# Kernel tuning notes

Measured on AMD Instinct MI355X. Metric: run time of the kernel, lower is better.

The kernel has to match this reference:

```python
import jax, jax.numpy as jnp
import numpy as np

B, N, F, UNITS = 8, 4096, 128, 64
NEG = -1e10
LEAKY_SLOPE = 0.2  # tf.nn.leaky_relu default


def setup_inputs() -> dict:
    key = jax.random.key(0)
    k1, k2, k3, k4, k5 = jax.random.split(key, 5)
    H = jax.random.normal(k1, (B, N, F), dtype=jnp.float32)
    A = jax.random.randint(k2, (B, N, N), 0, 2).astype(jnp.float32)
    # self-loops so every row has at least one unmasked entry
    A = jnp.maximum(A, jnp.eye(N, dtype=jnp.float32)[None])
    W = jax.random.normal(k3, (F, UNITS), dtype=jnp.float32) * (1.0 / np.sqrt(F))
    a_1 = jax.random.normal(k4, (UNITS, 1), dtype=jnp.float32) * (1.0 / np.sqrt(UNITS))
    a_2 = jax.random.normal(k5, (UNITS, 1), dtype=jnp.float32) * (1.0 / np.sqrt(UNITS))
    return {"H": H, "A": A, "W": W, "a_1": a_1, "a_2": a_2}


def reference(H, A, W, a_1, a_2):
    X = H @ W                                  # [B, N, U]
    attn_self = X @ a_1                        # [B, N, 1]
    attn_neigh = X @ a_2                       # [B, N, 1]
    attention = attn_self + jnp.swapaxes(attn_neigh, 1, 2)   # [B, N, N]
    E = jax.nn.leaky_relu(attention, negative_slope=LEAKY_SLOPE)
    masked_E = E + NEG * (1.0 - A)
    alpha = jax.nn.softmax(masked_E, axis=-1)  # row-wise softmax
    H_cap = alpha @ X                          # [B, N, U]
    return jax.nn.relu(H_cap)
```

## Files before the change

kernel.cpp:

```cpp
#include <hip/hip_runtime.h>
#include <hip/hip_bf16.h>


#define NTOK 4096
#define FDIM 128
#define UDIM 64
#define BATCH 8

typedef __attribute__((ext_vector_type(8))) short short8;
typedef __attribute__((ext_vector_type(4))) float f32x4;

__device__ __forceinline__ unsigned short f2bf(float x) {
    unsigned u = __float_as_uint(x);
    return (unsigned short)((u + 0x7fffu + ((u >> 16) & 1u)) >> 16);
}

__global__ __launch_bounds__(256) void prep_kernel(
    const float* __restrict__ H,
    const float* __restrict__ W,
    const float* __restrict__ a1,
    const float* __restrict__ a2,
    unsigned short* __restrict__ XT,
    float* __restrict__ s_out,
    float* __restrict__ t_out)
{
    __shared__ float Xl[4][16][UDIM + 1];

    const int tid  = threadIdx.x;
    const int wave = tid >> 6, lane = tid & 63;
    const int col  = lane & 15, quad = lane >> 4;
    const int i0   = (blockIdx.x * 4 + wave) * 16;

    f32x4 acc0 = {0,0,0,0}, acc1 = {0,0,0,0}, acc2 = {0,0,0,0}, acc3 = {0,0,0,0};
    const float* hrow = H + (size_t)(i0 + col) * FDIM + quad * 8;

    #pragma unroll
    for (int kb = 0; kb < FDIM; kb += 32) {
        f32x4 h0 = *(const f32x4*)(hrow + kb);
        f32x4 h1 = *(const f32x4*)(hrow + kb + 4);
        short8 afr, b0, b1, b2, b3;
        #pragma unroll
        for (int j = 0; j < 4; ++j) {
            afr[j]     = (short)f2bf(h0[j]);
            afr[4 + j] = (short)f2bf(h1[j]);
        }
        #pragma unroll
        for (int j = 0; j < 8; ++j) {
            int k = kb + quad * 8 + j;
            b0[j] = (short)f2bf(W[k * UDIM + col]);
            b1[j] = (short)f2bf(W[k * UDIM + 16 + col]);
            b2[j] = (short)f2bf(W[k * UDIM + 32 + col]);
            b3[j] = (short)f2bf(W[k * UDIM + 48 + col]);
        }
        acc0 = __builtin_amdgcn_mfma_f32_16x16x32_bf16(afr, b0, acc0, 0, 0, 0);
        acc1 = __builtin_amdgcn_mfma_f32_16x16x32_bf16(afr, b1, acc1, 0, 0, 0);
        acc2 = __builtin_amdgcn_mfma_f32_16x16x32_bf16(afr, b2, acc2, 0, 0, 0);
        acc3 = __builtin_amdgcn_mfma_f32_16x16x32_bf16(afr, b3, acc3, 0, 0, 0);
    }
    #pragma unroll
    for (int r = 0; r < 4; ++r) {
        Xl[wave][quad * 4 + r][col]      = acc0[r];
        Xl[wave][quad * 4 + r][16 + col] = acc1[r];
        Xl[wave][quad * 4 + r][32 + col] = acc2[r];
        Xl[wave][quad * 4 + r][48 + col] = acc3[r];
    }
    __syncthreads();

    const int b = i0 >> 12, n0 = i0 & (NTOK - 1);
    float ps = 0.f, pt = 0.f;
    #pragma unroll
    for (int ui = 0; ui < 16; ++ui) {
        int u = quad * 16 + ui;
        float x = Xl[wave][col][u];
        ps = fmaf(x, a1[u], ps);
        pt = fmaf(x, a2[u], pt);
    }
    ps += __shfl_xor(ps, 16, 64); ps += __shfl_xor(ps, 32, 64);
    pt += __shfl_xor(pt, 16, 64); pt += __shfl_xor(pt, 32, 64);
    if (quad == 0) s_out[i0 + col] = ps;
    if (quad == 1) t_out[i0 + col] = pt;

    #pragma unroll
    for (int ui = 0; ui < 16; ++ui) {
        int u = quad * 16 + ui;
        XT[(size_t)(b * UDIM + u) * NTOK + n0 + col] = f2bf(Xl[wave][col][u]);
    }
}

__global__ __launch_bounds__(256) void attn_kernel(
    const float* __restrict__ A,
    const unsigned short* __restrict__ XT,
    const float* __restrict__ s_in,
    const float* __restrict__ t_in,
    float* __restrict__ out)
{
    __shared__ float part[4][16][UDIM + 1];
    __shared__ float denl[4][16];

    const int tid  = threadIdx.x;
    const int wave = tid >> 6, lane = tid & 63;
    const int bx   = blockIdx.x;
    const int b    = bx & 7;
    const int i0   = (bx >> 3) * 16;
    const int col  = lane & 15, quad = lane >> 4;
    const int kstart = wave * (NTOK / 4);

    const float s_m = s_in[b * NTOK + i0 + col];

    const float* aptr = A + ((size_t)(b * NTOK + i0 + col)) * NTOK + kstart + quad * 8;
    const float* tptr = t_in + b * NTOK + kstart + quad * 8;
    const unsigned short* xb  = XT + (size_t)b * UDIM * NTOK + kstart + quad * 8;
    const unsigned short* xp0 = xb + (size_t)(col)      * NTOK;
    const unsigned short* xp1 = xb + (size_t)(16 + col) * NTOK;
    const unsigned short* xp2 = xb + (size_t)(32 + col) * NTOK;
    const unsigned short* xp3 = xb + (size_t)(48 + col) * NTOK;

    f32x4 acc0 = {0,0,0,0}, acc1 = {0,0,0,0}, acc2 = {0,0,0,0}, acc3 = {0,0,0,0};
    float den = 0.f;
    const float LOG2E = 1.44269504f;

    #pragma unroll 2
    for (int step = 0; step < 32; ++step) {
        f32x4 am0 = __builtin_nontemporal_load((const f32x4*)aptr);
        f32x4 am1 = __builtin_nontemporal_load((const f32x4*)(aptr + 4));
        f32x4 t0  = *(const f32x4*)tptr;
        f32x4 t1  = *(const f32x4*)(tptr + 4);
        short8 bf0 = *(const short8*)xp0;
        short8 bf1 = *(const short8*)xp1;
        short8 bf2 = *(const short8*)xp2;
        short8 bf3 = *(const short8*)xp3;

        float w[8];
        #pragma unroll
        for (int j = 0; j < 4; ++j) {
            float l0 = s_m + t0[j], l1 = s_m + t1[j];
            float e0 = fmaxf(l0, 0.2f * l0);
            float e1 = fmaxf(l1, 0.2f * l1);
            float w0 = __builtin_amdgcn_exp2f(e0 * LOG2E) * am0[j];
            float w1 = __builtin_amdgcn_exp2f(e1 * LOG2E) * am1[j];
            den += w0 + w1;
            w[j] = w0; w[4 + j] = w1;
        }
        short8 afr;
        #pragma unroll
        for (int j = 0; j < 4; ++j) {
            afr[j]     = (short)f2bf(w[j]);
            afr[4 + j] = (short)f2bf(w[4 + j]);
        }

        acc0 = __builtin_amdgcn_mfma_f32_16x16x32_bf16(afr, bf0, acc0, 0, 0, 0);
        acc1 = __builtin_amdgcn_mfma_f32_16x16x32_bf16(afr, bf1, acc1, 0, 0, 0);
        acc2 = __builtin_amdgcn_mfma_f32_16x16x32_bf16(afr, bf2, acc2, 0, 0, 0);
        acc3 = __builtin_amdgcn_mfma_f32_16x16x32_bf16(afr, bf3, acc3, 0, 0, 0);

        aptr += 32; tptr += 32; xp0 += 32; xp1 += 32; xp2 += 32; xp3 += 32;
    }

    den += __shfl_xor(den, 16, 64);
    den += __shfl_xor(den, 32, 64);
    if (quad == 0) denl[wave][col] = den;

    #pragma unroll
    for (int r = 0; r < 4; ++r) {
        part[wave][quad * 4 + r][col]      = acc0[r];
        part[wave][quad * 4 + r][16 + col] = acc1[r];
        part[wave][quad * 4 + r][32 + col] = acc2[r];
        part[wave][quad * 4 + r][48 + col] = acc3[r];
    }
    __syncthreads();

    #pragma unroll
    for (int rep = 0; rep < 4; ++rep) {
        int e = rep * 256 + tid;
        int r = e >> 6, u = e & 63;
        float num = part[0][r][u] + part[1][r][u] + part[2][r][u] + part[3][r][u];
        float dd  = denl[0][r] + denl[1][r] + denl[2][r] + denl[3][r];
        float o   = fmaxf(num / dd, 0.f);
        __builtin_nontemporal_store(o, &out[(size_t)(b * NTOK + i0 + r) * UDIM + u]);
    }
}

extern "C" void kernel_launch(void* const* d_in, const int* in_sizes, int n_in,
                              void* d_out, int out_size, void* d_ws, size_t ws_size,
                              hipStream_t stream) {
    const float* H  = (const float*)d_in[0];
    const float* A  = (const float*)d_in[1];
    const float* W  = (const float*)d_in[2];
    const float* a1 = (const float*)d_in[3];
    const float* a2 = (const float*)d_in[4];
    float* out = (float*)d_out;

    char* ws = (char*)d_ws;
    unsigned short* XT = (unsigned short*)ws;
    float* s = (float*)(ws + (size_t)BATCH * UDIM * NTOK * 2);
    float* t = (float*)(ws + (size_t)BATCH * UDIM * NTOK * 2 + (size_t)BATCH * NTOK * 4);

    prep_kernel<<<512, 256, 0, stream>>>(H, W, a1, a2, XT, s, t);
    attn_kernel<<<2048, 256, 0, stream>>>(A, XT, s, t, out);
}
```

Baseline: 782.5 us.

## Process 64 query rows per block to reuse X tiles across row groups

Each attention block now handles four 16-row groups (64 rows) instead of one, so every bf16 XT fragment and t vector loaded is reused across four MFMA row groups. Grid size drops from 2048 to 512 blocks. LOG2E is folded into s and t in the prep kernel, and the bf16 conversion is replaced with a cheaper add-and-byte-perm pack that rounds half up rather than to even. The trade-off is far more accumulator registers and shared memory per block, plus fewer blocks to hide the latency of streaming A.

```diff
diff --git a/kernel.cpp b/kernel.cpp
--- a/kernel.cpp
+++ b/kernel.cpp
@@ -9,6 +9,8 @@
 
 typedef __attribute__((ext_vector_type(8))) short short8;
 typedef __attribute__((ext_vector_type(4))) float f32x4;
+
+union PackU { unsigned u[4]; short8 s; };
 
 __device__ __forceinline__ unsigned short f2bf(float x) {
     unsigned u = __float_as_uint(x);
@@ -77,8 +79,9 @@
     }
     ps += __shfl_xor(ps, 16, 64); ps += __shfl_xor(ps, 32, 64);
     pt += __shfl_xor(pt, 16, 64); pt += __shfl_xor(pt, 32, 64);
-    if (quad == 0) s_out[i0 + col] = ps;
-    if (quad == 1) t_out[i0 + col] = pt;
+    const float LOG2E = 1.44269504f;
+    if (quad == 0) s_out[i0 + col] = ps * LOG2E;
+    if (quad == 1) t_out[i0 + col] = pt * LOG2E;
 
     #pragma unroll
     for (int ui = 0; ui < 16; ++ui) {
@@ -94,20 +97,25 @@
     const float* __restrict__ t_in,
     float* __restrict__ out)
 {
-    __shared__ float part[4][16][UDIM + 1];
-    __shared__ float denl[4][16];
+    __shared__ float part[4][64][UDIM + 1];
+    __shared__ float denl[4][64];
 
     const int tid  = threadIdx.x;
     const int wave = tid >> 6, lane = tid & 63;
     const int bx   = blockIdx.x;
     const int b    = bx & 7;
-    const int i0   = (bx >> 3) * 16;
+    const int i0   = (bx >> 3) * 64;
     const int col  = lane & 15, quad = lane >> 4;
     const int kstart = wave * (NTOK / 4);
 
-    const float s_m = s_in[b * NTOK + i0 + col];
-
-    const float* aptr = A + ((size_t)(b * NTOK + i0 + col)) * NTOK + kstart + quad * 8;
+    float s_m[4];
+    #pragma unroll
+    for (int g = 0; g < 4; ++g) s_m[g] = s_in[b * NTOK + i0 + g * 16 + col];
+
+    const float* ap[4];
+    #pragma unroll
+    for (int g = 0; g < 4; ++g)
+        ap[g] = A + ((size_t)(b * NTOK + i0 + g * 16 + col)) * NTOK + kstart + quad * 8;
     const float* tptr = t_in + b * NTOK + kstart + quad * 8;
     const unsigned short* xb  = XT + (size_t)b * UDIM * NTOK + kstart + quad * 8;
     const unsigned short* xp0 = xb + (size_t)(col)      * NTOK;
@@ -115,62 +123,70 @@
     const unsigned short* xp2 = xb + (size_t)(32 + col) * NTOK;
     const unsigned short* xp3 = xb + (size_t)(48 + col) * NTOK;
 
-    f32x4 acc0 = {0,0,0,0}, acc1 = {0,0,0,0}, acc2 = {0,0,0,0}, acc3 = {0,0,0,0};
-    float den = 0.f;
-    const float LOG2E = 1.44269504f;
+    f32x4 acc[4][4];
+    #pragma unroll
+    for (int g = 0; g < 4; ++g)
+        #pragma unroll
+        for (int f = 0; f < 4; ++f) acc[g][f] = (f32x4){0,0,0,0};
+    float den[4] = {0.f, 0.f, 0.f, 0.f};
 
     #pragma unroll 2
     for (int step = 0; step < 32; ++step) {
-        f32x4 am0 = __builtin_nontemporal_load((const f32x4*)aptr);
-        f32x4 am1 = __builtin_nontemporal_load((const f32x4*)(aptr + 4));
-        f32x4 t0  = *(const f32x4*)tptr;
-        f32x4 t1  = *(const f32x4*)(tptr + 4);
         short8 bf0 = *(const short8*)xp0;
         short8 bf1 = *(const short8*)xp1;
         short8 bf2 = *(const short8*)xp2;
         short8 bf3 = *(const short8*)xp3;
-
-        float w[8];
-        #pragma unroll
-        for (int j = 0; j < 4; ++j) {
-            float l0 = s_m + t0[j], l1 = s_m + t1[j];
-            float e0 = fmaxf(l0, 0.2f * l0);
-            float e1 = fmaxf(l1, 0.2f * l1);
-            float w0 = __builtin_amdgcn_exp2f(e0 * LOG2E) * am0[j];
-            float w1 = __builtin_amdgcn_exp2f(e1 * LOG2E) * am1[j];
-            den += w0 + w1;
-            w[j] = w0; w[4 + j] = w1;
-        }
-        short8 afr;
-        #pragma unroll
-        for (int j = 0; j < 4; ++j) {
-            afr[j]     = (short)f2bf(w[j]);
-            afr[4 + j] = (short)f2bf(w[4 + j]);
-        }
-
-        acc0 = __builtin_amdgcn_mfma_f32_16x16x32_bf16(afr, bf0, acc0, 0, 0, 0);
-        acc1 = __builtin_amdgcn_mfma_f32_16x16x32_bf16(afr, bf1, acc1, 0, 0, 0);
-        acc2 = __builtin_amdgcn_mfma_f32_16x16x32_bf16(afr, bf2, acc2, 0, 0, 0);
-        acc3 = __builtin_amdgcn_mfma_f32_16x16x32_bf16(afr, bf3, acc3, 0, 0, 0);
-
-        aptr += 32; tptr += 32; xp0 += 32; xp1 += 32; xp2 += 32; xp3 += 32;
-    }
-
-    den += __shfl_xor(den, 16, 64);
-    den += __shfl_xor(den, 32, 64);
-    if (quad == 0) denl[wave][col] = den;
-
-    #pragma unroll
-    for (int r = 0; r < 4; ++r) {
-        part[wave][quad * 4 + r][col]      = acc0[r];
-        part[wave][quad * 4 + r][16 + col] = acc1[r];
-        part[wave][quad * 4 + r][32 + col] = acc2[r];
-        part[wave][quad * 4 + r][48 + col] = acc3[r];
+        f32x4 t0  = *(const f32x4*)tptr;
+        f32x4 t1  = *(const f32x4*)(tptr + 4);
+
+        #pragma unroll
+        for (int g = 0; g < 4; ++g) {
+            f32x4 am0 = __builtin_nontemporal_load((const f32x4*)ap[g]);
+            f32x4 am1 = __builtin_nontemporal_load((const f32x4*)(ap[g] + 4));
+            unsigned uw[8];
+            #pragma unroll
+            for (int j = 0; j < 4; ++j) {
+                float l0 = s_m[g] + t0[j], l1 = s_m[g] + t1[j];
+                float e0 = fmaxf(l0, 0.2f * l0);
+                float e1 = fmaxf(l1, 0.2f * l1);
+                float w0 = __builtin_amdgcn_exp2f(e0) * am0[j];
+                float w1 = __builtin_amdgcn_exp2f(e1) * am1[j];
+                den[g] += w0 + w1;
+                uw[j]     = __float_as_uint(w0) + 0x8000u;
+                uw[4 + j] = __float_as_uint(w1) + 0x8000u;
+            }
+            PackU p;
+            p.u[0] = __builtin_amdgcn_perm(uw[1], uw[0], 0x07060302u);
+            p.u[1] = __builtin_amdgcn_perm(uw[3], uw[2], 0x07060302u);
+            p.u[2] = __builtin_amdgcn_perm(uw[5], uw[4], 0x07060302u);
+            p.u[3] = __builtin_amdgcn_perm(uw[7], uw[6], 0x07060302u);
+
+            acc[g][0] = __builtin_amdgcn_mfma_f32_16x16x32_bf16(p.s, bf0, acc[g][0], 0, 0, 0);
+            acc[g][1] = __builtin_amdgcn_mfma_f32_16x16x32_bf16(p.s, bf1, acc[g][1], 0, 0, 0);
+            acc[g][2] = __builtin_amdgcn_mfma_f32_16x16x32_bf16(p.s, bf2, acc[g][2], 0, 0, 0);
+            acc[g][3] = __builtin_amdgcn_mfma_f32_16x16x32_bf16(p.s, bf3, acc[g][3], 0, 0, 0);
+            ap[g] += 32;
+        }
+        tptr += 32; xp0 += 32; xp1 += 32; xp2 += 32; xp3 += 32;
+    }
+
+    #pragma unroll
+    for (int g = 0; g < 4; ++g) {
+        den[g] += __shfl_xor(den[g], 16, 64);
+        den[g] += __shfl_xor(den[g], 32, 64);
+        if (quad == 0) denl[wave][g * 16 + col] = den[g];
+        #pragma unroll
+        for (int r = 0; r < 4; ++r) {
+            part[wave][g * 16 + quad * 4 + r][col]      = acc[g][0][r];
+            part[wave][g * 16 + quad * 4 + r][16 + col] = acc[g][1][r];
+            part[wave][g * 16 + quad * 4 + r][32 + col] = acc[g][2][r];
+            part[wave][g * 16 + quad * 4 + r][48 + col] = acc[g][3][r];
+        }
     }
     __syncthreads();
 
     #pragma unroll
-    for (int rep = 0; rep < 4; ++rep) {
+    for (int rep = 0; rep < 16; ++rep) {
         int e = rep * 256 + tid;
         int r = e >> 6, u = e & 63;
         float num = part[0][r][u] + part[1][r][u] + part[2][r][u] + part[3][r][u];
@@ -196,5 +212,5 @@
     float* t = (float*)(ws + (size_t)BATCH * UDIM * NTOK * 2 + (size_t)BATCH * NTOK * 4);
 
     prep_kernel<<<512, 256, 0, stream>>>(H, W, a1, a2, XT, s, t);
-    attn_kernel<<<2048, 256, 0, stream>>>(A, XT, s, t, out);
-}
+    attn_kernel<<<512, 256, 0, stream>>>(A, XT, s, t, out);
+}
```

Result: faster. 739.9 us (-5.4%).

## Give each wave full rows, prefetch A, fold log2e and cheapen bf16 packing

Applied to the files above, without the earlier changes.

Work is split differently. Each wave now owns 16 distinct rows and walks the full 4096-column reduction, instead of four waves splitting the columns of the same 16 rows. This drops the shared-memory partial-sum combine and the barrier, and the grid shrinks to 512 blocks. The A tile is software-prefetched one step ahead with normal loads instead of nontemporal ones. log2(e) is folded into s and t in the prep kernel, and bf16 packing switches to an add-and-perm truncation, which changes rounding slightly (ties no longer round to even). Fewer blocks and longer serial loops per wave may lower memory-level parallelism on this bandwidth-bound A stream.

```diff
diff --git a/kernel.cpp b/kernel.cpp
--- a/kernel.cpp
+++ b/kernel.cpp
@@ -9,6 +9,8 @@
 
 typedef __attribute__((ext_vector_type(8))) short short8;
 typedef __attribute__((ext_vector_type(4))) float f32x4;
+
+union PackU { unsigned u[4]; short8 s; };
 
 __device__ __forceinline__ unsigned short f2bf(float x) {
     unsigned u = __float_as_uint(x);
@@ -77,8 +79,9 @@
     }
     ps += __shfl_xor(ps, 16, 64); ps += __shfl_xor(ps, 32, 64);
     pt += __shfl_xor(pt, 16, 64); pt += __shfl_xor(pt, 32, 64);
-    if (quad == 0) s_out[i0 + col] = ps;
-    if (quad == 1) t_out[i0 + col] = pt;
+    const float LOG2E = 1.44269504f;
+    if (quad == 0) s_out[i0 + col] = ps * LOG2E;
+    if (quad == 1) t_out[i0 + col] = pt * LOG2E;
 
     #pragma unroll
     for (int ui = 0; ui < 16; ++ui) {
@@ -94,22 +97,18 @@
     const float* __restrict__ t_in,
     float* __restrict__ out)
 {
-    __shared__ float part[4][16][UDIM + 1];
-    __shared__ float denl[4][16];
-
     const int tid  = threadIdx.x;
     const int wave = tid >> 6, lane = tid & 63;
     const int bx   = blockIdx.x;
     const int b    = bx & 7;
-    const int i0   = (bx >> 3) * 16;
+    const int i0   = (bx >> 3) * 64 + wave * 16;
     const int col  = lane & 15, quad = lane >> 4;
-    const int kstart = wave * (NTOK / 4);
 
     const float s_m = s_in[b * NTOK + i0 + col];
 
-    const float* aptr = A + ((size_t)(b * NTOK + i0 + col)) * NTOK + kstart + quad * 8;
-    const float* tptr = t_in + b * NTOK + kstart + quad * 8;
-    const unsigned short* xb  = XT + (size_t)b * UDIM * NTOK + kstart + quad * 8;
+    const float* aptr = A + ((size_t)(b * NTOK + i0 + col)) * NTOK + quad * 8;
+    const float* tptr = t_in + b * NTOK + quad * 8;
+    const unsigned short* xb  = XT + (size_t)b * UDIM * NTOK + quad * 8;
     const unsigned short* xp0 = xb + (size_t)(col)      * NTOK;
     const unsigned short* xp1 = xb + (size_t)(16 + col) * NTOK;
     const unsigned short* xp2 = xb + (size_t)(32 + col) * NTOK;
@@ -117,12 +116,18 @@
 
     f32x4 acc0 = {0,0,0,0}, acc1 = {0,0,0,0}, acc2 = {0,0,0,0}, acc3 = {0,0,0,0};
     float den = 0.f;
-    const float LOG2E = 1.44269504f;
 
-    #pragma unroll 2
-    for (int step = 0; step < 32; ++step) {
-        f32x4 am0 = __builtin_nontemporal_load((const f32x4*)aptr);
-        f32x4 am1 = __builtin_nontemporal_load((const f32x4*)(aptr + 4));
+    f32x4 pa0 = *(const f32x4*)aptr;
+    f32x4 pa1 = *(const f32x4*)(aptr + 4);
+
+    #pragma unroll 4
+    for (int step = 0; step < 128; ++step) {
+        f32x4 am0 = pa0, am1 = pa1;
+        if (step < 127) {
+            aptr += 32;
+            pa0 = *(const f32x4*)aptr;
+            pa1 = *(const f32x4*)(aptr + 4);
+        }
         f32x4 t0  = *(const f32x4*)tptr;
         f32x4 t1  = *(const f32x4*)(tptr + 4);
         short8 bf0 = *(const short8*)xp0;
@@ -130,53 +135,44 @@
         short8 bf2 = *(const short8*)xp2;
         short8 bf3 = *(const short8*)xp3;
 
-        float w[8];
+        unsigned uw[8];
         #pragma unroll
         for (int j = 0; j < 4; ++j) {
             float l0 = s_m + t0[j], l1 = s_m + t1[j];
             float e0 = fmaxf(l0, 0.2f * l0);
             float e1 = fmaxf(l1, 0.2f * l1);
-            float w0 = __builtin_amdgcn_exp2f(e0 * LOG2E) * am0[j];
-            float w1 = __builtin_amdgcn_exp2f(e1 * LOG2E) * am1[j];
+            float w0 = __builtin_amdgcn_exp2f(e0) * am0[j];
+            float w1 = __builtin_amdgcn_exp2f(e1) * am1[j];
             den += w0 + w1;
-            w[j] = w0; w[4 + j] = w1;
+            uw[j]     = __float_as_uint(w0) + 0x8000u;
+            uw[4 + j] = __float_as_uint(w1) + 0x8000u;
         }
-        short8 afr;
-        #pragma unroll
-        for (int j = 0; j < 4; ++j) {
-            afr[j]     = (short)f2bf(w[j]);
-            afr[4 + j] = (short)f2bf(w[4 + j]);
-        }
+        PackU p;
+        p.u[0] = __builtin_amdgcn_perm(uw[1], uw[0], 0x07060302u);
+        p.u[1] = __builtin_amdgcn_perm(uw[3], uw[2], 0x07060302u);
+        p.u[2] = __builtin_amdgcn_perm(uw[5], uw[4], 0x07060302u);
+        p.u[3] = __builtin_amdgcn_perm(uw[7], uw[6], 0x07060302u);
 
-        acc0 = __builtin_amdgcn_mfma_f32_16x16x32_bf16(afr, bf0, acc0, 0, 0, 0);
-        acc1 = __builtin_amdgcn_mfma_f32_16x16x32_bf16(afr, bf1, acc1, 0, 0, 0);
-        acc2 = __builtin_amdgcn_mfma_f32_16x16x32_bf16(afr, bf2, acc2, 0, 0, 0);
-        acc3 = __builtin_amdgcn_mfma_f32_16x16x32_bf16(afr, bf3, acc3, 0, 0, 0);
+        acc0 = __builtin_amdgcn_mfma_f32_16x16x32_bf16(p.s, bf0, acc0, 0, 0, 0);
+        acc1 = __builtin_amdgcn_mfma_f32_16x16x32_bf16(p.s, bf1, acc1, 0, 0, 0);
+        acc2 = __builtin_amdgcn_mfma_f32_16x16x32_bf16(p.s, bf2, acc2, 0, 0, 0);
+        acc3 = __builtin_amdgcn_mfma_f32_16x16x32_bf16(p.s, bf3, acc3, 0, 0, 0);
 
-        aptr += 32; tptr += 32; xp0 += 32; xp1 += 32; xp2 += 32; xp3 += 32;
+        tptr += 32; xp0 += 32; xp1 += 32; xp2 += 32; xp3 += 32;
     }
 
     den += __shfl_xor(den, 16, 64);
     den += __shfl_xor(den, 32, 64);
-    if (quad == 0) denl[wave][col] = den;
 
     #pragma unroll
     for (int r = 0; r < 4; ++r) {
-        part[wave][quad * 4 + r][col]      = acc0[r];
-        part[wave][quad * 4 + r][16 + col] = acc1[r];
-        part[wave][quad * 4 + r][32 + col] = acc2[r];
-        part[wave][quad * 4 + r][48 + col] = acc3[r];
-    }
-    __syncthreads();
-
-    #pragma unroll
-    for (int rep = 0; rep < 4; ++rep) {
-        int e = rep * 256 + tid;
-        int r = e >> 6, u = e & 63;
-        float num = part[0][r][u] + part[1][r][u] + part[2][r][u] + part[3][r][u];
-        float dd  = denl[0][r] + denl[1][r] + denl[2][r] + denl[3][r];
-        float o   = fmaxf(num / dd, 0.f);
-        __builtin_nontemporal_store(o, &out[(size_t)(b * NTOK + i0 + r) * UDIM + u]);
+        float dd = __shfl(den, quad * 4 + r, 64);
+        float inv = 1.0f / dd;
+        size_t o = (size_t)(b * NTOK + i0 + quad * 4 + r) * UDIM;
+        __builtin_nontemporal_store(fmaxf(acc0[r] * inv, 0.f), &out[o + col]);
+        __builtin_nontemporal_store(fmaxf(acc1[r] * inv, 0.f), &out[o + 16 + col]);
+        __builtin_nontemporal_store(fmaxf(acc2[r] * inv, 0.f), &out[o + 32 + col]);
+        __builtin_nontemporal_store(fmaxf(acc3[r] * inv, 0.f), &out[o + 48 + col]);
     }
 }
 
@@ -196,5 +192,5 @@
     float* t = (float*)(ws + (size_t)BATCH * UDIM * NTOK * 2 + (size_t)BATCH * NTOK * 4);
 
     prep_kernel<<<512, 256, 0, stream>>>(H, W, a1, a2, XT, s, t);
-    attn_kernel<<<2048, 256, 0, stream>>>(A, XT, s, t, out);
+    attn_kernel<<<512, 256, 0, stream>>>(A, XT, s, t, out);
 }
```

Result: no change. 778.1 us (-0.6%).
